# Kernel optimization log

Hardware: AMD Instinct MI355X
Metric: run time of the kernel (lower is better)

## Reference

```python
import jax, jax.numpy as jnp
import numpy as np

B, L, N, FA, FB, D, OUT, R, T = 128, 128, 6, 39, 10, 200, 1, 3, 2
MB = 256  # num bonds per molecule
NEG = -9e8


def setup_inputs():
    key = jax.random.key(0)
    ks = iter(jax.random.split(key, 64))
    def rn(shape, sc=0.05):
        return jax.random.normal(next(ks), shape, dtype=jnp.float32) * sc
    inp = {}
    inp['atom_list'] = jax.random.normal(next(ks), (B, L, FA), dtype=jnp.float32)
    inp['bond_list'] = jax.random.normal(next(ks), (B, MB, FB), dtype=jnp.float32)
    inp['atom_degree_list'] = jax.random.randint(next(ks), (B, L, N), 0, L, dtype=jnp.int32)
    inp['bond_degree_list'] = jax.random.randint(next(ks), (B, L, N), 0, MB, dtype=jnp.int32)
    inp['atom_mask'] = jnp.ones((B, L), dtype=jnp.float32)
    # parameters (torch Linear: y = x @ W + b with W stored here as [in, out])
    inp['W_atom'] = rn((FA, D)); inp['b_atom'] = rn((D,))
    inp['W_nei'] = rn((FA + FB, D)); inp['b_nei'] = rn((D,))
    inp['W_align'] = rn((R, 2 * D, 1)); inp['b_align'] = rn((R, 1))
    inp['W_attend'] = rn((R, D, D)); inp['b_attend'] = rn((R, D))
    # GRUCell weights, torch layout [3D, D], gate order r,z,n
    inp['Wih'] = rn((R, 3 * D, D)); inp['Whh'] = rn((R, 3 * D, D))
    inp['bih'] = rn((R, 3 * D)); inp['bhh'] = rn((R, 3 * D))
    inp['W_mol_align'] = rn((2 * D, 1)); inp['b_mol_align'] = rn((1,))
    inp['W_mol_attend'] = rn((D, D)); inp['b_mol_attend'] = rn((D,))
    inp['mWih'] = rn((3 * D, D)); inp['mWhh'] = rn((3 * D, D))
    inp['mbih'] = rn((3 * D,)); inp['mbhh'] = rn((3 * D,))
    inp['W_metric'] = rn((2 * D, D)); inp['b_metric'] = rn((D,))
    inp['W_out'] = rn((D, OUT)); inp['b_out'] = rn((OUT,))
    return inp


def _gather(feat, idx):
    # feat [B, M, F], idx [B, L, N] -> [B, L, N, F]
    b, l, n = idx.shape
    g = jnp.take_along_axis(feat, idx.reshape(b, l * n)[..., None], axis=1)
    return g.reshape(b, l, n, feat.shape[-1])


def _gru(x, h, Wih, Whh, bih, bhh):
    gi = x @ Wih.T + bih
    gh = h @ Whh.T + bhh
    ir, iz, inn = jnp.split(gi, 3, axis=-1)
    hr, hz, hn = jnp.split(gh, 3, axis=-1)
    r = jax.nn.sigmoid(ir + hr)
    z = jax.nn.sigmoid(iz + hz)
    n = jnp.tanh(inn + r * hn)
    return (1.0 - z) * n + z * h


def reference(atom_list, bond_list, atom_degree_list, bond_degree_list, atom_mask,
              W_atom, b_atom, W_nei, b_nei, W_align, b_align, W_attend, b_attend,
              Wih, Whh, bih, bhh, W_mol_align, b_mol_align, W_mol_attend, b_mol_attend,
              mWih, mWhh, mbih, mbhh, W_metric, b_metric, W_out, b_out):
    lrelu = jax.nn.leaky_relu
    b, l, _ = atom_list.shape
    atom_feature = lrelu(atom_list @ W_atom + b_atom)          # [B,L,D]
    atom_nei = _gather(atom_list, atom_degree_list)            # [B,L,N,FA]
    bond_nei = _gather(bond_list, bond_degree_list)            # [B,L,N,FB]
    nei = lrelu(jnp.concatenate([atom_nei, bond_nei], -1) @ W_nei + b_nei)  # [B,L,N,D]

    pad = (atom_degree_list == l - 1)
    attend_mask = (~pad).astype(jnp.float32)[..., None]        # [B,L,N,1]
    softmax_mask = jnp.where(pad, NEG, 0.0)[..., None]         # [B,L,N,1]

    h = atom_feature
    cur = atom_feature
    for r in range(R):
        if r > 0:
            nei = _gather(cur, atom_degree_list)
        exp = jnp.broadcast_to(cur[:, :, None, :], nei.shape)
        align = lrelu(jnp.concatenate([exp, nei], -1) @ W_align[r] + b_align[r])
        w = jax.nn.softmax(align + softmax_mask, axis=-2) * attend_mask
        trans = nei @ W_attend[r] + b_attend[r]
        ctx = jax.nn.elu(jnp.sum(w * trans, axis=-2))          # [B,L,D]
        h = _gru(ctx.reshape(-1, D), h.reshape(-1, D), Wih[r], Whh[r], bih[r], bhh[r]).reshape(b, l, D)
        cur = jax.nn.relu(h)

    am = atom_mask[..., None]                                   # [B,L,1]
    mol_feature = jnp.sum(cur * am, axis=-2)                    # [B,D]
    act_mol = jax.nn.relu(mol_feature)
    mol_softmax_mask = jnp.where(am == 0.0, NEG, 0.0)           # [B,L,1]
    for _ in range(T):
        exp = jnp.broadcast_to(act_mol[:, None, :], cur.shape)
        score = lrelu(jnp.concatenate([exp, cur], -1) @ W_mol_align + b_mol_align)
        w = jax.nn.softmax(score + mol_softmax_mask, axis=-2) * am
        trans = cur @ W_mol_attend + b_mol_attend
        ctx = jax.nn.elu(jnp.sum(w * trans, axis=-2))           # [B,D]
        mol_feature = _gru(ctx, mol_feature, mWih, mWhh, mbih, mbhh)
        act_mol = jax.nn.relu(mol_feature)

    dd = jnp.float32(R - 2)  # leaked python loop var `d` in the original
    feat = jnp.concatenate([mol_feature, mol_feature + dd], -1)
    return (feat @ W_metric + b_metric) @ W_out + b_out


if __name__ == '__main__':
    out = reference(**setup_inputs())
    print(out.shape)
```

## Files before the change

kernel.cpp:

```cpp
#include <hip/hip_runtime.h>
#include <hip/hip_bf16.h>
#include <math.h>
#include <string.h>

#define B_ 128
#define L_ 128
#define N_ 6
#define FA_ 39
#define FB_ 10
#define D_ 200
#define MB_ 256
#define R_ 3
#define T_ 2
#define NEGV -9e8f
#define BL_ (B_*L_)
#define G3D_ (3*D_)
#define FP32TAG 0x3F800000u
#define KP 416
#define NP 896
#define NP2 1024
#define KC 224
#define NC 256

typedef __hip_bfloat16 bf16;
typedef __attribute__((ext_vector_type(8))) short short8;
typedef __attribute__((ext_vector_type(4))) float f32x4;

__device__ __forceinline__ float b2f(const bf16 x){ return __bfloat162float(x); }
__device__ __forceinline__ unsigned short f2b(float v){ bf16 t = __float2bfloat16(v); return *reinterpret_cast<unsigned short*>(&t); }
__device__ __forceinline__ float bu2f(unsigned short u){ unsigned x = ((unsigned)u)<<16; float f; memcpy(&f,&x,4); return f; }
__device__ __forceinline__ float lo2f(unsigned x){ unsigned y = x<<16; float f; memcpy(&f,&y,4); return f; }
__device__ __forceinline__ float hi2f(unsigned x){ unsigned y = x & 0xffff0000u; float f; memcpy(&f,&y,4); return f; }
__device__ __forceinline__ float lreluf(float x){ return x>=0.f ? x : 0.01f*x; }
__device__ __forceinline__ float eluf(float x){ return x>0.f ? x : expm1f(x); }
__device__ __forceinline__ float sigmf(float x){ return 1.f/(1.f+expf(-x)); }

#define NSEG 14
struct CvtArgs { const void* src[NSEG]; int ofs[NSEG+1]; };

#define PREPB_N (R_*NP2*KP)
#define PREPW_N (R_*NC*KC)
#define PREPM_N (D_*G3D_)
#define PREPG_N (2*PREPM_N)
#define PREPT_N 40000
#define PREPE_N 80000
#define CONV_N 23989
#define XHPAD_N (BL_*16)
#define CPAD_N (BL_*24)
#define AROWS (BL_ + B_*MB_)
#define A_N (AROWS*64)
#define BI_N (448*64)

struct PrepArgs {
    CvtArgs cvt;
    const void *Wih, *Whh, *Watt, *mWih, *mWhh, *Wmt, *Wme;
    const void *bond, *Wnei, *atom, *Watom;
    float* conv;
    unsigned short *B2t, *WatT, *WGi, *WGh, *WmtT, *WmeT, *XH, *A16, *Bi16, *cur16;
    const unsigned* amtag;
    int ew_total;
};

__device__ __forceinline__ float ldd(const void* p, size_t i, bool f32){
    return f32 ? ((const float*)p)[i] : b2f(((const bf16*)p)[i]);
}

__global__ void __launch_bounds__(256) k_prep(PrepArgs A){
    bool f32 = (*A.amtag == FP32TAG);
    int i = blockIdx.x*256 + (int)threadIdx.x;
    if (i >= A.ew_total) return;
    if (i < CONV_N){
        int s = 0;
        while (i >= A.cvt.ofs[s+1]) s++;
        A.conv[i] = ldd(A.cvt.src[s], i - A.cvt.ofs[s], f32);
        return;
    }
    int i2 = i - CONV_N;
    if (i2 < PREPB_N){
        int kk = i2 % KP;
        int rest = i2 / KP;
        int c = rest % NP2;
        int r = rest / NP2;
        int g = c >> 8, n = c & 255;
        float v = 0.f;
        if (n < 200){
            if (g <= 1){
                int j = g*200 + n;
                if (kk < 200) v = ldd(A.Wih, ((size_t)(r*G3D_ + j))*D_ + kk, f32);
                else if (kk < 400) v = ldd(A.Whh, ((size_t)(r*G3D_ + j))*D_ + (kk-200), f32);
            } else if (g == 2){
                if (kk < 200) v = ldd(A.Wih, ((size_t)(r*G3D_ + 400 + n))*D_ + kk, f32);
            } else {
                if (kk >= 200 && kk < 400) v = ldd(A.Whh, ((size_t)(r*G3D_ + 400 + n))*D_ + (kk-200), f32);
            }
        }
        A.B2t[i2] = f2b(v);
        return;
    }
    int i3 = i2 - PREPB_N;
    if (i3 < PREPW_N){
        int kk = i3 % KC;
        int rest = i3 / KC;
        int n = rest % NC;
        int r = rest / NC;
        float v = 0.f;
        if (kk < 200 && n < 200) v = ldd(A.Watt, ((size_t)r*D_ + kk)*D_ + n, f32);
        A.WatT[i3] = f2b(v);
        return;
    }
    int i4 = i3 - PREPW_N;
    if (i4 < PREPG_N){
        int half = i4 / PREPM_N;
        int s = i4 - half*PREPM_N;
        (half ? A.WGh : A.WGi)[s] = f2b(ldd(half ? A.mWhh : A.mWih, s, f32));
        return;
    }
    int i5 = i4 - PREPG_N;
    if (i5 < PREPT_N){
        int k = i5 / 200, d = i5 % 200;
        A.WmtT[(size_t)d*200 + k] = f2b(ldd(A.Wmt, i5, f32));
        return;
    }
    int i6 = i5 - PREPT_N;
    if (i6 < PREPE_N){
        int k = i6 / 200, d = i6 % 200;
        A.WmeT[(size_t)d*400 + k] = f2b(ldd(A.Wme, i6, f32));
        return;
    }
    int i7 = i6 - PREPE_N;
    if (i7 < XHPAD_N){
        int al = i7 >> 4, j = i7 & 15;
        A.XH[(size_t)al*KP + 400 + j] = 0;
        return;
    }
    int i7b = i7 - XHPAD_N;
    if (i7b < CPAD_N){
        int al = i7b / 24, j = i7b % 24;
        A.cur16[(size_t)al*KC + 200 + j] = 0;
        return;
    }
    int i8 = i7b - CPAD_N;
    if (i8 < A_N){
        int row = i8 >> 6, k = i8 & 63;
        float v = 0.f;
        if (row < BL_){
            if (k < FA_) v = ldd(A.atom, (size_t)row*FA_ + k, f32);
        } else {
            int rb = row - BL_;
            if (k >= FA_ && k < FA_+FB_) v = ldd(A.bond, (size_t)rb*FB_ + (k-FA_), f32);
        }
        A.A16[i8] = f2b(v);
        return;
    }
    int i9 = i8 - A_N;
    if (i9 < BI_N){
        int n = i9 >> 6, k = i9 & 63;
        float v = 0.f;
        if (n < 200){
            if (k < FA_) v = ldd(A.Watom, (size_t)k*D_ + n, f32);
        } else if (n < 400){
            if (k < FA_+FB_) v = ldd(A.Wnei, (size_t)k*D_ + (n-200), f32);
        }
        A.Bi16[i9] = f2b(v);
    }
}

__global__ void __launch_bounds__(256) k_initmm(const unsigned short* __restrict__ A16,
        const unsigned short* __restrict__ Bi16,
        const void* __restrict__ batom, const void* __restrict__ bnei,
        unsigned short* __restrict__ XH, unsigned short* __restrict__ P16,
        unsigned short* __restrict__ Q16, const unsigned* __restrict__ amtag){
    __shared__ unsigned short As[128][40];
    __shared__ unsigned short Bs[64][40];
    bool f32 = (*amtag == FP32TAG);
    int tid = threadIdx.x;
    int mt = (int)blockIdx.x / 7, nt = (int)blockIdx.x % 7;
    int m0 = mt*128, n0 = nt*64;
    if (m0 >= BL_ && n0 + 64 <= 200) return;
    int lane = tid & 63, wv = tid >> 6;
    int quad = lane >> 4, lm = lane & 15;
    f32x4 acc[2][4];
    #pragma unroll
    for (int a=0;a<2;a++)
        #pragma unroll
        for (int b=0;b<4;b++) acc[a][b] = (f32x4){0.f,0.f,0.f,0.f};
    for (int ks = 0; ks < 2; ks++){
        int r0_ = tid >> 2, c0 = (tid & 3) * 8;
        int r1_ = (tid + 256) >> 2, c1 = ((tid + 256) & 3) * 8;
        uint4 a0 = *(const uint4*)&A16[(size_t)(m0 + r0_)*64 + ks*32 + c0];
        uint4 a1 = *(const uint4*)&A16[(size_t)(m0 + r1_)*64 + ks*32 + c1];
        uint4 b0 = *(const uint4*)&Bi16[(size_t)(n0 + (tid >> 2))*64 + ks*32 + (tid & 3)*8];
        __syncthreads();
        *(uint4*)&As[r0_][c0] = a0;
        *(uint4*)&As[r1_][c1] = a1;
        *(uint4*)&Bs[tid >> 2][(tid & 3)*8] = b0;
        __syncthreads();
        short8 av0 = *(const short8*)&As[wv*32 + lm][quad*8];
        short8 av1 = *(const short8*)&As[wv*32 + 16 + lm][quad*8];
        #pragma unroll
        for (int ns=0; ns<4; ns++){
            short8 bv = *(const short8*)&Bs[ns*16 + lm][quad*8];
            acc[0][ns] = __builtin_amdgcn_mfma_f32_16x16x32_bf16(av0, bv, acc[0][ns], 0,0,0);
            acc[1][ns] = __builtin_amdgcn_mfma_f32_16x16x32_bf16(av1, bv, acc[1][ns], 0,0,0);
        }
    }
    #pragma unroll
    for (int ms=0; ms<2; ms++)
      #pragma unroll
      for (int ns=0; ns<4; ns++){
        int n = n0 + ns*16 + lm;
        #pragma unroll
        for (int i=0;i<4;i++){
            int row = m0 + wv*32 + ms*16 + quad*4 + i;
            float v = acc[ms][ns][i];
            if (row < BL_){
                if (n < 200){
                    XH[(size_t)row*KP + 200 + n] = f2b(lreluf(v + ldd(batom, n, f32)));
                } else if (n < 400){
                    P16[(size_t)row*D_ + (n-200)] = f2b(v + ldd(bnei, n-200, f32));
                }
            } else if (n >= 200 && n < 400){
                Q16[(size_t)(row-BL_)*D_ + (n-200)] = f2b(v);
            }
        }
      }
}

__global__ void __launch_bounds__(256) k_attn(
        const unsigned short* __restrict__ cur16, const unsigned short* __restrict__ XH,
        const float* __restrict__ s1, const float* __restrict__ tb,
        const int* __restrict__ adl, const int* __restrict__ bdl,
        const unsigned short* __restrict__ P16, const unsigned short* __restrict__ Q16,
        const float* __restrict__ W_align, const float* __restrict__ b_align, int r,
        unsigned short* __restrict__ wnei, float* __restrict__ wsum){
    int bid = blockIdx.x;
    int mol = bid & (B_-1), chunk = bid >> 7;
    int wv = threadIdx.x >> 6, lane = threadIdx.x & 63;
    int al = mol*L_ + chunk*4 + wv;
    __shared__ float s_nei[4][N_][D_];

    int idxn[N_]; bool pad[N_];
    #pragma unroll
    for (int n=0;n<N_;n++){ idxn[n] = adl[al*N_ + n]; pad[n] = (idxn[n] == L_-1); }

    float s2[N_];
    float s1v;
    if (r == 0){
        const float* Wab = W_align + D_;
        float acc[N_+1];
        #pragma unroll
        for (int n=0;n<N_+1;n++) acc[n] = 0.f;
        #pragma unroll
        for (int n=0;n<N_;n++){
            int bd = bdl[al*N_ + n];
            const unsigned short* Prow = P16 + ((size_t)mol*L_ + idxn[n])*D_;
            const unsigned short* Qrow = Q16 + ((size_t)mol*MB_ + bd)*D_;
            for (int d=lane; d<D_; d+=64){
                float v = lreluf(bu2f(Prow[d]) + bu2f(Qrow[d]));
                s_nei[wv][n][d] = v;
                acc[n] += v * Wab[d];
            }
        }
        for (int d=lane; d<D_; d+=64)
            acc[N_] += bu2f(XH[(size_t)al*KP + 200 + d]) * W_align[d];
        #pragma unroll
        for (int o=32;o>0;o>>=1)
            #pragma unroll
            for (int n=0;n<N_+1;n++) acc[n] += __shfl_xor(acc[n],o);
        #pragma unroll
        for (int n=0;n<N_;n++) s2[n] = acc[n];
        s1v = acc[N_];
    } else {
        float tmp = 0.f;
        if (lane < N_) tmp = tb[mol*L_ + idxn[lane]];
        #pragma unroll
        for (int n=0;n<N_;n++) s2[n] = __shfl(tmp, n);
        s1v = s1[al];
    }

    float bav = b_align[r];
    float a[N_]; float mx = -1e30f;
    #pragma unroll
    for (int n=0;n<N_;n++){
        float v = lreluf(s1v + s2[n] + bav);
        if (pad[n]) v += NEGV;
        a[n] = v; mx = fmaxf(mx, v);
    }
    float w[N_]; float se = 0.f;
    #pragma unroll
    for (int n=0;n<N_;n++){ float e = expf(a[n]-mx); w[n]=e; se += e; }
    float inv = 1.f/se; float wsv = 0.f;
    #pragma unroll
    for (int n=0;n<N_;n++){ w[n] = pad[n] ? 0.f : w[n]*inv; wsv += w[n]; }

    if (r == 0){
        for (int d=lane; d<D_; d+=64){
            float acc = 0.f;
            #pragma unroll
            for (int n=0;n<N_;n++) acc += w[n] * s_nei[wv][n][d];
            wnei[(size_t)al*KC + d] = f2b(acc);
        }
    } else {
        for (int d=lane; d<D_; d+=64){
            float acc = 0.f;
            #pragma unroll
            for (int n=0;n<N_;n++) acc += w[n] * bu2f(cur16[((size_t)mol*L_ + idxn[n])*KC + d]);
            wnei[(size_t)al*KC + d] = f2b(acc);
        }
    }
    if (lane < 24) wnei[(size_t)al*KC + 200 + lane] = 0;
    if (lane==0) wsum[al] = wsv;
}

__global__ void __launch_bounds__(256) k_ctxmfma(const unsigned short* __restrict__ Wn,
        const float* __restrict__ wsum, const unsigned short* __restrict__ WatT,
        const float* __restrict__ bias, int r, unsigned short* __restrict__ XH,
        float* __restrict__ s1, float* __restrict__ tb, float* __restrict__ curdot){
    __shared__ unsigned short As[128][40];
    __shared__ unsigned short Bs[64][40];
    int tid = threadIdx.x;
    int m0 = ((int)blockIdx.x & 127) * 128;
    int n0 = ((int)blockIdx.x >> 7) * 64;
    if (n0 == 0 && tid < 128){
        int row = m0 + tid;
        s1[row] = 0.f; tb[row] = 0.f;
        if (r == R_-1) curdot[row] = 0.f;
        #pragma unroll
        for (int j=0;j<16;j++) XH[(size_t)row*KP + 400 + j] = 0;
    }
    const unsigned short* Bt = WatT + (size_t)r*NC*KC;
    int lane = tid & 63, wv = tid >> 6;
    int quad = lane >> 4, lm = lane & 15;
    f32x4 acc[2][4];
    #pragma unroll
    for (int a=0;a<2;a++)
        #pragma unroll
        for (int b=0;b<4;b++) acc[a][b] = (f32x4){0.f,0.f,0.f,0.f};
    for (int ks = 0; ks < 7; ks++){
        int r0_ = tid >> 2, c0 = (tid & 3) * 8;
        int r1_ = (tid + 256) >> 2, c1 = ((tid + 256) & 3) * 8;
        uint4 a0 = *(const uint4*)&Wn[(size_t)(m0 + r0_)*KC + ks*32 + c0];
        uint4 a1 = *(const uint4*)&Wn[(size_t)(m0 + r1_)*KC + ks*32 + c1];
        uint4 b0 = *(const uint4*)&Bt[(size_t)(n0 + (tid >> 2))*KC + ks*32 + (tid & 3)*8];
        __syncthreads();
        *(uint4*)&As[r0_][c0] = a0;
        *(uint4*)&As[r1_][c1] = a1;
        *(uint4*)&Bs[tid >> 2][(tid & 3)*8] = b0;
        __syncthreads();
        short8 av0 = *(const short8*)&As[wv*32 + lm][quad*8];
        short8 av1 = *(const short8*)&As[wv*32 + 16 + lm][quad*8];
        #pragma unroll
        for (int ns=0; ns<4; ns++){
            short8 bv = *(const short8*)&Bs[ns*16 + lm][quad*8];
            acc[0][ns] = __builtin_amdgcn_mfma_f32_16x16x32_bf16(av0, bv, acc[0][ns], 0,0,0);
            acc[1][ns] = __builtin_amdgcn_mfma_f32_16x16x32_bf16(av1, bv, acc[1][ns], 0,0,0);
        }
    }
    #pragma unroll
    for (int ms=0; ms<2; ms++)
      #pragma unroll
      for (int ns=0; ns<4; ns++){
        int n = n0 + ns*16 + lm;
        if (n < 200){
            float bv = bias[r*D_ + n];
            #pragma unroll
            for (int i=0;i<4;i++){
                int row = m0 + wv*32 + ms*16 + quad*4 + i;
                float v = acc[ms][ns][i] + wsum[row]*bv;
                XH[(size_t)row*KP + n] = f2b(eluf(v));
            }
        }
      }
}

__global__ void __launch_bounds__(512, 1) k_gemm2(
        const unsigned short* __restrict__ XHr, unsigned short* __restrict__ XHw,
        const unsigned short* __restrict__ B2t, unsigned short* __restrict__ cur16,
        const float* __restrict__ bih, const float* __restrict__ bhh,
        const float* __restrict__ W_align, const float* __restrict__ Wma,
        float* __restrict__ s1, float* __restrict__ tb, float* __restrict__ curdot,
        int r){
    __shared__ unsigned short As[128][40];
    __shared__ unsigned short Bs[512][40];
    __shared__ float s_ab[4][128][2];
    int tid = threadIdx.x;
    int m0 = ((int)blockIdx.x & 127) * 128;
    int half = (int)blockIdx.x >> 7;
    const unsigned short* Bt = B2t + (size_t)r*NP2*KP;
    int lane = tid & 63, wv = tid >> 6;
    int wm = wv >> 2, wn = wv & 3;
    int quad = lane >> 4, lm = lane & 15;
    f32x4 acc[4][8];
    #pragma unroll
    for (int a=0;a<4;a++)
        #pragma unroll
        for (int b=0;b<8;b++) acc[a][b] = (f32x4){0.f,0.f,0.f,0.f};
    int ar = tid >> 2, ac = (tid & 3) * 8;
    for (int ks = 0; ks < 13; ks++){
        uint4 a0 = *(const uint4*)&XHr[(size_t)(m0 + ar)*KP + ks*32 + ac];
        uint4 bq[4];
        #pragma unroll
        for (int q=0;q<4;q++)
            bq[q] = *(const uint4*)&Bt[(size_t)(q*256 + half*128 + ar)*KP + ks*32 + ac];
        __syncthreads();
        *(uint4*)&As[ar][ac] = a0;
        #pragma unroll
        for (int q=0;q<4;q++) *(uint4*)&Bs[ar + 128*q][ac] = bq[q];
        __syncthreads();
        short8 av[4];
        #pragma unroll
        for (int mm=0;mm<4;mm++) av[mm] = *(const short8*)&As[wm*64 + mm*16 + lm][quad*8];
        #pragma unroll
        for (int jp=0; jp<8; jp++){
            int lf = wn + 4*jp;
            short8 bv = *(const short8*)&Bs[lf*16 + lm][quad*8];
            #pragma unroll
            for (int mm=0;mm<4;mm++)
                acc[mm][jp] = __builtin_amdgcn_mfma_f32_16x16x32_bf16(av[mm], bv, acc[mm][jp], 0,0,0);
        }
    }
    if (tid < 128){
        #pragma unroll
        for (int q=0;q<4;q++){ s_ab[q][tid][0] = 0.f; s_ab[q][tid][1] = 0.f; }
    }
    __syncthreads();
    const float* bi = bih + r*G3D_;
    const float* bh = bhh + r*G3D_;
    const float* Wa = W_align + (r+1)*2*D_;
    bool last = (r == R_-1);
    #pragma unroll
    for (int mm=0; mm<4; mm++){
        float pa[4] = {0.f,0.f,0.f,0.f}, pb[4] = {0.f,0.f,0.f,0.f};
        #pragma unroll
        for (int jj=0; jj<2; jj++){
            int d = half*128 + (wn + 4*jj)*16 + lm;
            if (d < 200){
                float bir=bi[d], biz=bi[D_+d], bin=bi[2*D_+d];
                float bhr=bh[d], bhz=bh[D_+d], bhn=bh[2*D_+d];
                float wa1 = last ? Wma[D_+d] : Wa[d];
                float wa2 = last ? 0.f : Wa[D_+d];
                #pragma unroll
                for (int i=0;i<4;i++){
                    int row = m0 + wm*64 + mm*16 + quad*4 + i;
                    float rsum = acc[mm][0+jj][i];
                    float zsum = acc[mm][2+jj][i];
                    float gin  = acc[mm][4+jj][i];
                    float ghn  = acc[mm][6+jj][i];
                    float rr = sigmf(rsum + bir + bhr);
                    float zz = sigmf(zsum + biz + bhz);
                    float nn = tanhf(gin + bin + rr*(ghn + bhn));
                    size_t hx = (size_t)row*KP + 200 + d;
                    float hv = bu2f(XHr[hx]);
                    float hn = (1.f-zz)*nn + zz*hv;
                    XHw[hx] = f2b(hn);
                    float cv = fmaxf(hn, 0.f);
                    cur16[(size_t)row*KC + d] = f2b(cv);
                    pa[i] += cv * wa1;
                    pb[i] += cv * wa2;
                }
            }
        }
        #pragma unroll
        for (int o=1;o<16;o<<=1){
            #pragma unroll
            for (int i=0;i<4;i++){ pa[i] += __shfl_xor(pa[i],o); pb[i] += __shfl_xor(pb[i],o); }
        }
        if (lm == 0){
            #pragma unroll
            for (int i=0;i<4;i++){
                int lr = wm*64 + mm*16 + quad*4 + i;
                s_ab[wn][lr][0] = pa[i];
                s_ab[wn][lr][1] = pb[i];
            }
        }
    }
    __syncthreads();
    if (tid < 128){
        int row = m0 + tid;
        float a1 = (s_ab[0][tid][0] + s_ab[1][tid][0]) + (s_ab[2][tid][0] + s_ab[3][tid][0]);
        float a2 = (s_ab[0][tid][1] + s_ab[1][tid][1]) + (s_ab[2][tid][1] + s_ab[3][tid][1]);
        if (last) atomicAdd(&curdot[row], a1);
        else { atomicAdd(&s1[row], a1); atomicAdd(&tb[row], a2); }
    }
}

__device__ __forceinline__ float brSum(float v, float* s_red){
    for (int o=32;o>0;o>>=1) v += __shfl_xor(v,o);
    int lane = threadIdx.x & 63, wid = threadIdx.x >> 6;
    __syncthreads();
    if (lane==0) s_red[wid] = v;
    __syncthreads();
    float r = 0.f;
    int nw = blockDim.x >> 6;
    for (int i=0;i<nw;i++) r += s_red[i];
    return r;
}

__device__ __forceinline__ float dot200(const unsigned short* __restrict__ wrow,
                                        const float* __restrict__ v){
    const uint4* wp = (const uint4*)wrow;
    float a0=0.f, a1=0.f;
    #pragma unroll
    for (int kk=0; kk<25; kk++){
        uint4 u = wp[kk];
        f32x4 A = *(const f32x4*)&v[8*kk];
        f32x4 Bv = *(const f32x4*)&v[8*kk+4];
        a0 += A[0]*lo2f(u.x) + A[1]*hi2f(u.x);
        a1 += A[2]*lo2f(u.y) + A[3]*hi2f(u.y);
        a0 += Bv[0]*lo2f(u.z) + Bv[1]*hi2f(u.z);
        a1 += Bv[2]*lo2f(u.w) + Bv[3]*hi2f(u.w);
    }
    return a0 + a1;
}

__global__ void __launch_bounds__(512, 1) k_mol(const unsigned short* __restrict__ cur16,
    const float* __restrict__ curdot, const float* __restrict__ atom_mask,
    const float* __restrict__ Wma, const float* __restrict__ bma,
    const unsigned short* __restrict__ WmtT, const float* __restrict__ bmt,
    const unsigned short* __restrict__ WGi, const unsigned short* __restrict__ WGh,
    const float* __restrict__ mbih, const float* __restrict__ mbhh,
    const unsigned short* __restrict__ WmeT, const float* __restrict__ bme,
    const float* __restrict__ Wout, const float* __restrict__ bout,
    void* __restrict__ out, const unsigned* __restrict__ amtag){
    int b = blockIdx.x, tid = threadIdx.x;
    int wv = tid >> 6, lane = tid & 63;
    int dq = tid & 255, cq = tid >> 8;
    __shared__ unsigned short s_cur[L_*KC];
    __shared__ float s_am[L_], s_neg[L_], s_cd[L_];
    __shared__ float s_wp[4][L_];
    __shared__ __attribute__((aligned(16))) float s_mf[D_];
    __shared__ __attribute__((aligned(16))) float s_act[D_];
    __shared__ __attribute__((aligned(16))) float s_wc[D_];
    __shared__ __attribute__((aligned(16))) float s_ctx[D_];
    __shared__ __attribute__((aligned(16))) float s_mf2[2*D_];
    __shared__ float s_gi[G3D_], s_gh[G3D_];
    __shared__ float s_wma[D_], s_bmt[D_], s_bi[G3D_], s_bh[G3D_];
    __shared__ float s_part[2][256];
    __shared__ float s_red[8];
    __shared__ float s_wsm;
    const uint4* src = (const uint4*)(cur16 + (size_t)b*L_*KC);
    for (int i = tid; i < L_*KC/8; i += 512) ((uint4*)s_cur)[i] = src[i];
    if (tid < L_){
        float am = atom_mask[b*L_ + tid];
        s_am[tid] = am;
        s_neg[tid] = (am == 0.f) ? NEGV : 0.f;
        s_cd[tid] = curdot[b*L_ + tid];
    }
    if (tid < D_){ s_wma[tid] = Wma[tid]; s_bmt[tid] = bmt[tid]; }
    for (int j = tid; j < G3D_; j += 512){
        s_bi[j] = mbih[j];
        s_bh[j] = mbhh[j];
    }
    __syncthreads();
    {
        float a0 = 0.f, a1 = 0.f;
        if (dq < D_)
            for (int l=cq*64; l<cq*64+64; l+=2){
                a0 += bu2f(s_cur[l*KC + dq]) * s_am[l];
                a1 += bu2f(s_cur[(l+1)*KC + dq]) * s_am[l+1];
            }
        s_part[cq][dq] = a0 + a1;
        __syncthreads();
        if (tid < D_){
            float v = s_part[0][tid] + s_part[1][tid];
            s_mf[tid] = v; s_act[tid] = fmaxf(v, 0.f);
        }
        __syncthreads();
    }
    float bma0 = bma[0];
    #pragma unroll 1
    for (int t=0;t<T_;t++){
        if (wv < 4){
            float a = s_act[lane]*s_wma[lane] + s_act[lane+64]*s_wma[lane+64];
            a += s_act[lane+128]*s_wma[lane+128];
            if (lane < 8) a += s_act[lane+192]*s_wma[lane+192];
            #pragma unroll
            for (int o=32;o>0;o>>=1) a += __shfl_xor(a,o);
            float sc0 = lreluf(a + s_cd[lane] + bma0) + s_neg[lane];
            float sc1 = lreluf(a + s_cd[lane+64] + bma0) + s_neg[lane+64];
            float m = fmaxf(sc0, sc1);
            #pragma unroll
            for (int o=32;o>0;o>>=1) m = fmaxf(m, __shfl_xor(m,o));
            float e0 = expf(sc0 - m), e1 = expf(sc1 - m);
            float s = e0 + e1;
            #pragma unroll
            for (int o=32;o>0;o>>=1) s += __shfl_xor(s,o);
            float inv = 1.f/s;
            float w0 = e0*inv*s_am[lane], w1 = e1*inv*s_am[lane+64];
            float ws = w0 + w1;
            #pragma unroll
            for (int o=32;o>0;o>>=1) ws += __shfl_xor(ws,o);
            s_wp[wv][lane] = w0; s_wp[wv][lane+64] = w1;
            if (tid == 0) s_wsm = ws;
            if (tid < D_){
                float acc = 0.f;
                #pragma unroll 16
                for (int l=0; l<L_; l++)
                    acc += s_wp[wv][l] * bu2f(s_cur[l*KC + tid]);
                s_wc[tid] = acc;
            }
        } else {
            int h = tid - 256;
            #pragma unroll 1
            for (int rr=0; rr<3; rr++){
                int row = h + rr*256;
                if (row < G3D_)
                    s_gh[row] = dot200(WGh + (size_t)row*D_, s_mf);
                __builtin_amdgcn_sched_barrier(0);
            }
        }
        __syncthreads();
        if (tid < D_){
            float acc = dot200(WmtT + (size_t)tid*D_, s_wc);
            s_ctx[tid] = eluf(acc + s_wsm * s_bmt[tid]);
        }
        __syncthreads();
        {
            #pragma unroll 1
            for (int rr=0; rr<2; rr++){
                int row = tid + rr*512;
                if (row < G3D_)
                    s_gi[row] = dot200(WGi + (size_t)row*D_, s_ctx);
                __builtin_amdgcn_sched_barrier(0);
            }
        }
        __syncthreads();
        if (tid < D_){
            int d = tid;
            float rr = sigmf(s_gi[d] + s_bi[d] + s_gh[d] + s_bh[d]);
            float zz = sigmf(s_gi[D_+d] + s_bi[D_+d] + s_gh[D_+d] + s_bh[D_+d]);
            float nn = tanhf(s_gi[2*D_+d] + s_bi[2*D_+d] + rr*(s_gh[2*D_+d] + s_bh[2*D_+d]));
            float nm = (1.f-zz)*nn + zz*s_mf[d];
            s_mf[d] = nm; s_act[d] = fmaxf(nm, 0.f);
        }
        __syncthreads();
        __builtin_amdgcn_sched_barrier(0);
    }
    const float dd = (float)(R_ - 2);
    if (tid < 2*D_) s_mf2[tid] = (tid < D_) ? s_mf[tid] : s_mf[tid - D_] + dd;
    __syncthreads();
    float p2 = 0.f;
    if (tid < D_){
        const uint4* wp = (const uint4*)(WmeT + (size_t)tid*400);
        float a0=0.f, a1=0.f;
        #pragma unroll
        for (int kk=0; kk<50; kk++){
            uint4 u = wp[kk];
            f32x4 wA = *(const f32x4*)&s_mf2[8*kk];
            f32x4 wB = *(const f32x4*)&s_mf2[8*kk+4];
            a0 += wA[0]*lo2f(u.x) + wA[1]*hi2f(u.x);
            a1 += wA[2]*lo2f(u.y) + wA[3]*hi2f(u.y);
            a0 += wB[0]*lo2f(u.z) + wB[1]*hi2f(u.z);
            a1 += wB[2]*lo2f(u.w) + wB[3]*hi2f(u.w);
        }
        p2 = (a0 + a1 + bme[tid]) * Wout[tid];
    }
    float o = brSum(p2, s_red);
    if (tid==0){
        o += bout[0];
        if (*amtag == FP32TAG) ((float*)out)[b] = o;
        else ((bf16*)out)[b] = __float2bfloat16(o);
    }
}

extern "C" void kernel_launch(void* const* d_in, const int* in_sizes, int n_in,
                              void* d_out, int out_size, void* d_ws, size_t ws_size,
                              hipStream_t stream) {
    const int* adl = (const int*)d_in[2];
    const int* bdl = (const int*)d_in[3];
    const unsigned* amtag = (const unsigned*)d_in[4];

    static const int srcidx[NSEG] = {4,9,10,12,15,16,17,18,20,23,24,26,27,28};
    static const int segsz[NSEG]  = {16384,1200,3,600,1800,1800,400,1,200,600,600,200,200,1};
    CvtArgs ca;
    int ofs[NSEG+1]; ofs[0] = 0;
    for (int i=0;i<NSEG;i++){ ca.src[i] = d_in[srcidx[i]]; ca.ofs[i] = ofs[i]; ofs[i+1] = ofs[i] + segsz[i]; }
    ca.ofs[NSEG] = ofs[NSEG];

    float* ws   = (float*)d_ws;
    float* conv = ws;
    unsigned short* XHa   = (unsigned short*)(conv + 24000);
    unsigned short* B2t   = XHa + (size_t)BL_*KP;
    unsigned short* WatT  = B2t + PREPB_N;
    unsigned short* WGi   = WatT + PREPW_N;
    unsigned short* WGh   = WGi + PREPM_N;
    unsigned short* WmtT  = WGh + PREPM_N;
    unsigned short* WmeT  = WmtT + PREPT_N;
    unsigned short* Bi16  = WmeT + PREPE_N;
    unsigned short* cur16 = Bi16 + BI_N;
    unsigned short* creg  = cur16 + (size_t)BL_*KC;
    unsigned short* A16  = creg;
    unsigned short* wnei = creg;
    unsigned short* Q16  = creg + (size_t)BL_*KC;
    unsigned short* P16  = Q16 + (size_t)B_*MB_*D_;
    unsigned short* XHb  = Q16;
    float* s1     = (float*)(creg + (size_t)BL_*NP);
    float* tb     = s1 + BL_;
    float* wsum   = tb + BL_;
    float* curdot = wsum + BL_;

    const float* c_amask = conv + ofs[0];
    const float* c_Walign= conv + ofs[1];
    const float* c_balign= conv + ofs[2];
    const float* c_batt  = conv + ofs[3];
    const float* c_bih   = conv + ofs[4];
    const float* c_bhh   = conv + ofs[5];
    const float* c_Wma   = conv + ofs[6];
    const float* c_bma   = conv + ofs[7];
    const float* c_bmt   = conv + ofs[8];
    const float* c_mbih  = conv + ofs[9];
    const float* c_mbhh  = conv + ofs[10];
    const float* c_bme   = conv + ofs[11];
    const float* c_Wout  = conv + ofs[12];
    const float* c_bout  = conv + ofs[13];

    PrepArgs A;
    A.cvt = ca;
    A.Wih = d_in[13]; A.Whh = d_in[14]; A.Watt = d_in[11];
    A.mWih = d_in[21]; A.mWhh = d_in[22]; A.Wmt = d_in[19]; A.Wme = d_in[25];
    A.bond = d_in[1]; A.Wnei = d_in[7]; A.atom = d_in[0]; A.Watom = d_in[5];
    A.conv = conv;
    A.B2t = B2t; A.WatT = WatT; A.WGi = WGi; A.WGh = WGh; A.WmtT = WmtT; A.WmeT = WmeT;
    A.XH = XHa; A.A16 = A16; A.Bi16 = Bi16; A.cur16 = cur16;
    A.amtag = amtag;
    A.ew_total = CONV_N + PREPB_N + PREPW_N + PREPG_N + PREPT_N + PREPE_N
               + XHPAD_N + CPAD_N + A_N + BI_N;

    k_prep<<<(A.ew_total + 255)/256, 256, 0, stream>>>(A);
    k_initmm<<<(AROWS/128)*7, 256, 0, stream>>>(A16, Bi16, d_in[6], d_in[8],
                                                XHa, P16, Q16, amtag);

    for (int r=0; r<R_; r++){
        unsigned short* XHr = (r & 1) ? XHb : XHa;
        unsigned short* XHw = (r & 1) ? XHa : XHb;
        k_attn<<<BL_/4, 256, 0, stream>>>(cur16, XHa, s1, tb, adl, bdl, P16, Q16,
                                          c_Walign, c_balign, r, wnei, wsum);
        k_ctxmfma<<<(BL_/128)*(NC/64), 256, 0, stream>>>(wnei, wsum, WatT, c_batt, r, XHr,
                                                         s1, tb, curdot);
        k_gemm2<<<256, 512, 0, stream>>>(XHr, XHw, B2t, cur16, c_bih, c_bhh,
                                         c_Walign, c_Wma, s1, tb, curdot, r);
    }

    k_mol<<<B_, 512, 0, stream>>>(cur16, curdot, c_amask, c_Wma, c_bma, WmtT, c_bmt,
                                  WGi, WGh, c_mbih, c_mbhh, WmeT, c_bme, c_Wout, c_bout,
                                  d_out, amtag);
}
```

Before: 452.1 us.

## Retile GRU gate GEMM into 512 blocks of 256 threads, 64 output columns each

The GRU gate GEMM kernel is retiled so each block covers 128 rows by 64 hidden columns (four gate groups) with 4 waves, launching 512 blocks of 256 threads instead of 256 blocks of 512. The per-row gate bias loads are hoisted out of the epilogue loop. The aim is more blocks per GPU and two blocks resident per CU, giving better occupancy and latency hiding. In exchange the A tile is reloaded by twice as many blocks, and the last column slice (d 192-255) is mostly padding, so some MFMA work is wasted.

```diff
diff --git a/kernel.cpp b/kernel.cpp
--- a/kernel.cpp
+++ b/kernel.cpp
@@ -373,7 +373,7 @@
       }
 }
 
-__global__ void __launch_bounds__(512, 1) k_gemm2(
+__global__ void __launch_bounds__(256, 2) k_gemm2(
         const unsigned short* __restrict__ XHr, unsigned short* __restrict__ XHw,
         const unsigned short* __restrict__ B2t, unsigned short* __restrict__ cur16,
         const float* __restrict__ bih, const float* __restrict__ bhh,
@@ -381,83 +381,79 @@
         float* __restrict__ s1, float* __restrict__ tb, float* __restrict__ curdot,
         int r){
     __shared__ unsigned short As[128][40];
-    __shared__ unsigned short Bs[512][40];
+    __shared__ unsigned short Bs[256][40];
     __shared__ float s_ab[4][128][2];
     int tid = threadIdx.x;
     int m0 = ((int)blockIdx.x & 127) * 128;
-    int half = (int)blockIdx.x >> 7;
+    int ds = (int)blockIdx.x >> 7;
     const unsigned short* Bt = B2t + (size_t)r*NP2*KP;
-    int lane = tid & 63, wv = tid >> 6;
-    int wm = wv >> 2, wn = wv & 3;
+    int lane = tid & 63, wn = tid >> 6;
     int quad = lane >> 4, lm = lane & 15;
-    f32x4 acc[4][8];
-    #pragma unroll
-    for (int a=0;a<4;a++)
-        #pragma unroll
-        for (int b=0;b<8;b++) acc[a][b] = (f32x4){0.f,0.f,0.f,0.f};
+    f32x4 acc[8][4];
+    #pragma unroll
+    for (int a=0;a<8;a++)
+        #pragma unroll
+        for (int b=0;b<4;b++) acc[a][b] = (f32x4){0.f,0.f,0.f,0.f};
     int ar = tid >> 2, ac = (tid & 3) * 8;
     for (int ks = 0; ks < 13; ks++){
         uint4 a0 = *(const uint4*)&XHr[(size_t)(m0 + ar)*KP + ks*32 + ac];
+        uint4 a1 = *(const uint4*)&XHr[(size_t)(m0 + 64 + ar)*KP + ks*32 + ac];
         uint4 bq[4];
         #pragma unroll
         for (int q=0;q<4;q++)
-            bq[q] = *(const uint4*)&Bt[(size_t)(q*256 + half*128 + ar)*KP + ks*32 + ac];
+            bq[q] = *(const uint4*)&Bt[(size_t)(q*256 + ds*64 + ar)*KP + ks*32 + ac];
         __syncthreads();
         *(uint4*)&As[ar][ac] = a0;
-        #pragma unroll
-        for (int q=0;q<4;q++) *(uint4*)&Bs[ar + 128*q][ac] = bq[q];
-        __syncthreads();
-        short8 av[4];
-        #pragma unroll
-        for (int mm=0;mm<4;mm++) av[mm] = *(const short8*)&As[wm*64 + mm*16 + lm][quad*8];
-        #pragma unroll
-        for (int jp=0; jp<8; jp++){
-            int lf = wn + 4*jp;
-            short8 bv = *(const short8*)&Bs[lf*16 + lm][quad*8];
-            #pragma unroll
-            for (int mm=0;mm<4;mm++)
-                acc[mm][jp] = __builtin_amdgcn_mfma_f32_16x16x32_bf16(av[mm], bv, acc[mm][jp], 0,0,0);
-        }
-    }
-    if (tid < 128){
-        #pragma unroll
-        for (int q=0;q<4;q++){ s_ab[q][tid][0] = 0.f; s_ab[q][tid][1] = 0.f; }
-    }
-    __syncthreads();
+        *(uint4*)&As[64 + ar][ac] = a1;
+        #pragma unroll
+        for (int q=0;q<4;q++) *(uint4*)&Bs[q*64 + ar][ac] = bq[q];
+        __syncthreads();
+        short8 bv[4];
+        #pragma unroll
+        for (int g=0;g<4;g++) bv[g] = *(const short8*)&Bs[g*64 + wn*16 + lm][quad*8];
+        #pragma unroll
+        for (int mm=0; mm<8; mm++){
+            short8 av = *(const short8*)&As[mm*16 + lm][quad*8];
+            #pragma unroll
+            for (int g=0;g<4;g++)
+                acc[mm][g] = __builtin_amdgcn_mfma_f32_16x16x32_bf16(av, bv[g], acc[mm][g], 0,0,0);
+        }
+    }
     const float* bi = bih + r*G3D_;
     const float* bh = bhh + r*G3D_;
     const float* Wa = W_align + (r+1)*2*D_;
     bool last = (r == R_-1);
-    #pragma unroll
-    for (int mm=0; mm<4; mm++){
+    int d = ds*64 + wn*16 + lm;
+    bool dok = (d < 200);
+    float bir=0.f,biz=0.f,bin=0.f,bhr=0.f,bhz=0.f,bhn=0.f,wa1=0.f,wa2=0.f;
+    if (dok){
+        bir=bi[d]; biz=bi[D_+d]; bin=bi[2*D_+d];
+        bhr=bh[d]; bhz=bh[D_+d]; bhn=bh[2*D_+d];
+        wa1 = last ? Wma[D_+d] : Wa[d];
+        wa2 = last ? 0.f : Wa[D_+d];
+    }
+    #pragma unroll
+    for (int mm=0; mm<8; mm++){
         float pa[4] = {0.f,0.f,0.f,0.f}, pb[4] = {0.f,0.f,0.f,0.f};
-        #pragma unroll
-        for (int jj=0; jj<2; jj++){
-            int d = half*128 + (wn + 4*jj)*16 + lm;
-            if (d < 200){
-                float bir=bi[d], biz=bi[D_+d], bin=bi[2*D_+d];
-                float bhr=bh[d], bhz=bh[D_+d], bhn=bh[2*D_+d];
-                float wa1 = last ? Wma[D_+d] : Wa[d];
-                float wa2 = last ? 0.f : Wa[D_+d];
-                #pragma unroll
-                for (int i=0;i<4;i++){
-                    int row = m0 + wm*64 + mm*16 + quad*4 + i;
-                    float rsum = acc[mm][0+jj][i];
-                    float zsum = acc[mm][2+jj][i];
-                    float gin  = acc[mm][4+jj][i];
-                    float ghn  = acc[mm][6+jj][i];
-                    float rr = sigmf(rsum + bir + bhr);
-                    float zz = sigmf(zsum + biz + bhz);
-                    float nn = tanhf(gin + bin + rr*(ghn + bhn));
-                    size_t hx = (size_t)row*KP + 200 + d;
-                    float hv = bu2f(XHr[hx]);
-                    float hn = (1.f-zz)*nn + zz*hv;
-                    XHw[hx] = f2b(hn);
-                    float cv = fmaxf(hn, 0.f);
-                    cur16[(size_t)row*KC + d] = f2b(cv);
-                    pa[i] += cv * wa1;
-                    pb[i] += cv * wa2;
-                }
+        if (dok){
+            #pragma unroll
+            for (int i=0;i<4;i++){
+                int row = m0 + mm*16 + quad*4 + i;
+                float rsum = acc[mm][0][i];
+                float zsum = acc[mm][1][i];
+                float gin  = acc[mm][2][i];
+                float ghn  = acc[mm][3][i];
+                float rr = sigmf(rsum + bir + bhr);
+                float zz = sigmf(zsum + biz + bhz);
+                float nn = tanhf(gin + bin + rr*(ghn + bhn));
+                size_t hx = (size_t)row*KP + 200 + d;
+                float hv = bu2f(XHr[hx]);
+                float hn = (1.f-zz)*nn + zz*hv;
+                XHw[hx] = f2b(hn);
+                float cv = fmaxf(hn, 0.f);
+                cur16[(size_t)row*KC + d] = f2b(cv);
+                pa[i] += cv * wa1;
+                pb[i] += cv * wa2;
             }
         }
         #pragma unroll
@@ -468,7 +464,7 @@
         if (lm == 0){
             #pragma unroll
             for (int i=0;i<4;i++){
-                int lr = wm*64 + mm*16 + quad*4 + i;
+                int lr = mm*16 + quad*4 + i;
                 s_ab[wn][lr][0] = pa[i];
                 s_ab[wn][lr][1] = pb[i];
             }
@@ -737,7 +733,7 @@
                                           c_Walign, c_balign, r, wnei, wsum);
         k_ctxmfma<<<(BL_/128)*(NC/64), 256, 0, stream>>>(wnei, wsum, WatT, c_batt, r, XHr,
                                                          s1, tb, curdot);
-        k_gemm2<<<256, 512, 0, stream>>>(XHr, XHw, B2t, cur16, c_bih, c_bhh,
+        k_gemm2<<<512, 256, 0, stream>>>(XHr, XHw, B2t, cur16, c_bih, c_bhh,
                                          c_Walign, c_Wma, s1, tb, curdot, r);
     }
 
```

After: 437.6 us. 1.03x faster.
